# Performance work log

Hardware: AMD Instinct MI355X
Metric: run time of the kernel (lower is better)

The kernel has to match this reference:

```python
import jax, jax.numpy as jnp
import numpy as np

B, S, H, D = 1, 8192, 16, 128
BS = 64            # sparse_block_size
NB = S // BS       # 128 blocks
NUM_ORACLES = 32
ORACLE = S // NUM_ORACLES          # 256
LOCAL = ORACLE // BS               # 4 sliding-window blocks
PATTERN_ID = 0


def _build_block_pattern():
    """Block-level mask exactly as DKernelPredefinedSparseAttention.create_mask((0,))."""
    qb = np.arange(NB)[:, None]
    kb = np.arange(NB)[None, :]
    causal = qb >= kb
    window = (qb - kb) < LOCAL
    vert = np.zeros(NB, dtype=bool)
    real_col = int(PATTERN_ID * ORACLE + 0.5)
    vert[real_col // BS:(real_col + ORACLE) // BS] = True
    vert[0:1] = True
    mask = causal & (window | vert[None, :])
    kmax = int(mask.sum(axis=1).max())  # = 8 for this pattern
    kidx = np.zeros((NB, kmax), dtype=np.int32)
    kvalid = np.zeros((NB, kmax), dtype=bool)
    for i in range(NB):
        idx = np.nonzero(mask[i])[0]
        kidx[i, :len(idx)] = idx
        kvalid[i, :len(idx)] = True
    return kidx, kvalid


def setup_inputs() -> dict:
    key = jax.random.key(0)
    kq, kk, kv = jax.random.split(key, 3)
    q = jax.random.normal(kq, (B, S, H, D), dtype=jnp.float32)
    k = jax.random.normal(kk, (B, S, H, D), dtype=jnp.float32)
    v = jax.random.normal(kv, (B, S, H, D), dtype=jnp.float32)
    kidx_np, kvalid_np = _build_block_pattern()
    return {"q": q, "k": k, "v": v,
            "kidx": jnp.asarray(kidx_np), "kvalid": jnp.asarray(kvalid_np)}


def reference(q, k, v, kidx, kvalid):
    # q,k,v: [B,S,H,D] (bshd). kidx/kvalid: [NB, Kmax] active k-block ids per q-block.
    b, s, h, d = q.shape
    nb = s // BS
    kmax = kidx.shape[1]
    qb = q.reshape(b, nb, BS, h, d)
    kb = k.reshape(b, nb, BS, h, d)
    vb = v.reshape(b, nb, BS, h, d)
    # Gather only active k/v blocks -> [B, nb, Kmax, BS, H, D]
    kg = kb[:, kidx]
    vg = vb[:, kidx]
    scale = 1.0 / jnp.sqrt(jnp.float32(d))
    # [B, H, nb, BS(q), Kmax, BS(k)]
    scores = jnp.einsum('bqahd,bqkchd->bhqakc', qb, kg) * scale
    # element-level causal mask within the block pattern
    qpos = jnp.arange(nb)[:, None] * BS + jnp.arange(BS)[None, :]          # [nb, BS]
    kpos = kidx[..., None] * BS + jnp.arange(BS)[None, None, :]            # [nb, Kmax, BS]
    allow = (qpos[:, :, None, None] >= kpos[:, None, :, :]) & kvalid[:, None, :, None]
    scores = jnp.where(allow[None, None], scores, jnp.float32(-1e30))
    probs = jax.nn.softmax(scores.reshape(b, h, nb, BS, kmax * BS), axis=-1)
    probs = probs.reshape(scores.shape)
    out = jnp.einsum('bhqakc,bqkchd->bqahd', probs, vg)
    return out.reshape(b, s, h, d)
```

## Files before the change

### kernel.cpp

```cpp
#include <hip/hip_runtime.h>
#include <hip/hip_bf16.h>

#define HH 16
#define DD 128
#define NBQ 128
#define SS 8192

typedef __attribute__((ext_vector_type(4))) float f32x4;
typedef __attribute__((ext_vector_type(4))) short bf16x4;
typedef __attribute__((ext_vector_type(8))) short bf16x8;

__device__ __forceinline__ short f2bf_hw(float f) {
  __hip_bfloat16 b = __float2bfloat16(f);
  return __builtin_bit_cast(short, b);
}

__device__ __forceinline__ void gload_lds16(const void* g, void* l) {
  __builtin_amdgcn_global_load_lds(
      (const __attribute__((address_space(1))) void*)g,
      (__attribute__((address_space(3))) void*)l, 16, 0, 0);
}

__global__ __launch_bounds__(256)
void conv_k_kernel(const float* __restrict__ kg, unsigned short* __restrict__ kb) {
  const size_t e = ((size_t)blockIdx.x * 256 + threadIdx.x) * 4;
  const int h = (int)(e >> 20);
  const int s = (int)((e >> 7) & (SS - 1));
  const int d = (int)(e & 127);
  f32x4 a = *(const f32x4*)(kg + ((size_t)s * HH + h) * DD + d);
  bf16x4 o;
  o[0] = f2bf_hw(a[0]); o[1] = f2bf_hw(a[1]);
  o[2] = f2bf_hw(a[2]); o[3] = f2bf_hw(a[3]);
  *(bf16x4*)(kb + e) = o;
}

__global__ __launch_bounds__(256)
void conv_vt2_kernel(const float* __restrict__ vg, unsigned short* __restrict__ vt) {
  __shared__ unsigned short tile[128 * 72];
  const int kb = blockIdx.x, h = blockIdx.y, tid = threadIdx.x;
  {
    const int r = tid >> 2, q = tid & 3;
    const float* vp = vg + ((size_t)(kb * 64 + r) * HH + h) * DD + q * 32;
    #pragma unroll
    for (int c = 0; c < 8; ++c) {
      f32x4 a = *(const f32x4*)(vp + c * 4);
      #pragma unroll
      for (int j = 0; j < 4; ++j)
        tile[(q * 32 + c * 4 + j) * 72 + r] = (unsigned short)f2bf_hw(a[j]);
    }
  }
  __syncthreads();
  const int d = tid >> 1, half = tid & 1;
  unsigned short* op = vt + ((size_t)(h * NBQ + kb) * 128 + d) * 64 + half * 32;
  #pragma unroll
  for (int j = 0; j < 4; ++j) {
    bf16x8 f;
    #pragma unroll
    for (int e = 0; e < 8; ++e) {
      const int p = half * 32 + j * 8 + e;
      const int key = ((p >> 2) & 3) * 16 + (p >> 4) * 4 + (p & 3);
      f[e] = (short)tile[d * 72 + key];
    }
    *(bf16x8*)(op + j * 8) = f;
  }
}

#define SWK(o) ((o) ^ ((((o) >> 8) & 7) << 4))
#define SWV(o) ((o) ^ ((((o) >> 7) & 7) << 4))

__global__ __launch_bounds__(512, 4)
void sparse_attn_v14(const float* __restrict__ qg_, const unsigned short* __restrict__ kbuf,
                     const unsigned short* __restrict__ vtbuf, float* __restrict__ outg) {
  extern __shared__ __align__(16) char lds[];

  const int bx   = blockIdx.x;
  const int w    = (bx & 7) * 128 + (bx >> 3);
  const int h    = w >> 6;
  const int qgrp = w & 63;
  const int tid  = threadIdx.x;
  const int wid  = tid >> 6;
  const int lane = tid & 63;
  const int l15  = lane & 15;
  const int lg   = lane >> 4;

  const int qlo  = qgrp * 2, qhi = qgrp * 2 + 1;
  const int qb_w = qlo + (wid >> 2);
  const int rib0 = (wid & 3) * 16;

  const int nv     = (qhi + 1 < 4) ? qhi + 1 : 4;
  const int wstart = (qlo - 3 > 4) ? qlo - 3 : 4;
  const int nw     = (qhi - wstart + 1 > 0) ? qhi - wstart + 1 : 0;
  const int nlist  = nv + nw;

  const float scale = 0.12752030522080552f;

  const int rowg = qgrp * 128 + (wid >> 2) * 64 + rib0;

  bf16x8 qa[4];
  {
    const float* qp = qg_ + ((size_t)(rowg + l15) * HH + h) * DD;
    #pragma unroll
    for (int kc = 0; kc < 4; ++kc) {
      const int d0 = kc * 32 + lg * 8;
      f32x4 a = *(const f32x4*)(qp + d0);
      f32x4 b = *(const f32x4*)(qp + d0 + 4);
      bf16x8 f;
      f[0] = f2bf_hw(a[0] * scale); f[1] = f2bf_hw(a[1] * scale);
      f[2] = f2bf_hw(a[2] * scale); f[3] = f2bf_hw(a[3] * scale);
      f[4] = f2bf_hw(b[0] * scale); f[5] = f2bf_hw(b[1] * scale);
      f[6] = f2bf_hw(b[2] * scale); f[7] = f2bf_hw(b[3] * scale);
      qa[kc] = f;
    }
  }

  f32x4 oa[8];
  #pragma unroll
  for (int i = 0; i < 8; ++i) oa[i] = (f32x4){0.f, 0.f, 0.f, 0.f};
  float mr = -1e30f;
  float lr = 0.f;

  const char* kbase = (const char*)kbuf + ((size_t)h * NBQ << 14);
  const char* vbase = (const char*)vtbuf + ((size_t)h * NBQ << 14);

  {
    #pragma unroll
    for (int p = 0; p < 2; ++p) {
      const int ob = p * 8192 + wid * 1024;
      const int o  = ob + lane * 16;
      gload_lds16(kbase + SWK(o), lds + ob);
      gload_lds16(vbase + SWV(o), lds + 16384 + ob);
    }
  }
  __syncthreads();

  for (int t = 0; t < nlist; ++t) {
    const int kb = (t < nv) ? t : (wstart + (t - nv));
    const bool valid = (kb <= qb_w) && ((qb_w - kb < 4) || (kb < 4));
    char* Vb = lds + 16384 + (t & 1) * 16384;
    const bool havenext = (t + 1 < nlist);
    const int kbn = havenext ? ((t + 1 < nv) ? (t + 1) : (wstart + (t + 1 - nv))) : 0;

    if (havenext) {
      const char* vsrc = vbase + ((size_t)kbn << 14);
      char* Vd = lds + 16384 + ((t + 1) & 1) * 16384;
      #pragma unroll
      for (int p = 0; p < 2; ++p) {
        const int ob = p * 8192 + wid * 1024;
        const int o  = ob + lane * 16;
        gload_lds16(vsrc + SWV(o), Vd + ob);
      }
    }

    f32x4 s[4];
    if (valid) {
      #pragma unroll
      for (int kt = 0; kt < 4; ++kt) s[kt] = (f32x4){0.f, 0.f, 0.f, 0.f};
      __builtin_amdgcn_s_setprio(1);
      #pragma unroll
      for (int kt = 0; kt < 4; ++kt) {
        const int key = kt * 16 + l15;
        #pragma unroll
        for (int kc = 0; kc < 4; ++kc) {
          const int off = (key * 256 + (kc * 32 + lg * 8) * 2) ^ ((key & 7) << 4);
          bf16x8 kf = *(const bf16x8*)(lds + off);
          s[kt] = __builtin_amdgcn_mfma_f32_16x16x32_bf16(kf, qa[kc], s[kt], 0, 0, 0);
        }
      }
      __builtin_amdgcn_s_setprio(0);
    }

    __syncthreads();

    if (havenext) {
      const char* ksrc = kbase + ((size_t)kbn << 14);
      #pragma unroll
      for (int p = 0; p < 2; ++p) {
        const int ob = p * 8192 + wid * 1024;
        const int o  = ob + lane * 16;
        gload_lds16(ksrc + SWK(o), lds + ob);
      }
    }

    if (valid) {
      if (kb == qb_w) {
        const int rib = rib0 + l15;
        #pragma unroll
        for (int kt = 0; kt < 4; ++kt)
          #pragma unroll
          for (int r = 0; r < 4; ++r) {
            const int key = kt * 16 + lg * 4 + r;
            if (rib < key) s[kt][r] = -1e30f;
          }
      }

      {
        float a0 = fmaxf(fmaxf(s[0][0], s[0][1]), fmaxf(s[0][2], s[0][3]));
        float a1 = fmaxf(fmaxf(s[1][0], s[1][1]), fmaxf(s[1][2], s[1][3]));
        float a2 = fmaxf(fmaxf(s[2][0], s[2][1]), fmaxf(s[2][2], s[2][3]));
        float a3 = fmaxf(fmaxf(s[3][0], s[3][1]), fmaxf(s[3][2], s[3][3]));
        float lanemax = fmaxf(fmaxf(a0, a1), fmaxf(a2, a3));
        if (!__all(lanemax <= mr + 8.f)) {
          float mx = lanemax;
          mx = fmaxf(mx, __shfl_xor(mx, 16));
          mx = fmaxf(mx, __shfl_xor(mx, 32));
          const float mnew = fmaxf(mr, mx);
          const float sc = __builtin_amdgcn_exp2f(mr - mnew);
          lr *= sc;
          mr = mnew;
          const float s0 = __shfl(sc, lg * 4 + 0);
          const float s1 = __shfl(sc, lg * 4 + 1);
          const float s2 = __shfl(sc, lg * 4 + 2);
          const float s3 = __shfl(sc, lg * 4 + 3);
          #pragma unroll
          for (int nd = 0; nd < 8; ++nd) {
            oa[nd][0] *= s0; oa[nd][1] *= s1;
            oa[nd][2] *= s2; oa[nd][3] *= s3;
          }
        }
        float lsum = 0.f;
        #pragma unroll
        for (int kt = 0; kt < 4; ++kt)
          #pragma unroll
          for (int r = 0; r < 4; ++r) {
            const float p = __builtin_amdgcn_exp2f(s[kt][r] - mr);
            s[kt][r] = p;
            lsum += p;
          }
        lr += lsum;
      }

      bf16x4 pa[4];
      #pragma unroll
      for (int kt = 0; kt < 4; ++kt) {
        unsigned u0 = (unsigned)(unsigned short)f2bf_hw(s[kt][0]) |
                      ((unsigned)(unsigned short)f2bf_hw(s[kt][1]) << 16);
        unsigned u1 = (unsigned)(unsigned short)f2bf_hw(s[kt][2]) |
                      ((unsigned)(unsigned short)f2bf_hw(s[kt][3]) << 16);
        uint2 uu; uu.x = u0; uu.y = u1;
        pa[kt] = __builtin_bit_cast(bf16x4, uu);
      }

      __builtin_amdgcn_s_setprio(1);
      #pragma unroll
      for (int nd = 0; nd < 8; ++nd) {
        const int d = nd * 16 + l15;
        #pragma unroll
        for (int hb = 0; hb < 2; ++hb) {
          const int off = (d * 128 + lg * 32 + hb * 16) ^ ((d & 7) << 4);
          bf16x8 v2 = *(const bf16x8*)(Vb + off);
          bf16x4 vlo = __builtin_shufflevector(v2, v2, 0, 1, 2, 3);
          bf16x4 vhi = __builtin_shufflevector(v2, v2, 4, 5, 6, 7);
          oa[nd] = __builtin_amdgcn_mfma_f32_16x16x16bf16_1k(pa[2 * hb],     vlo, oa[nd], 0, 0, 0);
          oa[nd] = __builtin_amdgcn_mfma_f32_16x16x16bf16_1k(pa[2 * hb + 1], vhi, oa[nd], 0, 0, 0);
        }
      }
      __builtin_amdgcn_s_setprio(0);
    }
    __syncthreads();
  }

  {
    float l = lr;
    l += __shfl_xor(l, 16);
    l += __shfl_xor(l, 32);
    const float inv = 1.0f / l;
    const float i0 = __shfl(inv, lg * 4 + 0);
    const float i1 = __shfl(inv, lg * 4 + 1);
    const float i2 = __shfl(inv, lg * 4 + 2);
    const float i3 = __shfl(inv, lg * 4 + 3);
    float* op = outg + ((size_t)rowg * HH + h) * DD;
    #pragma unroll
    for (int nd = 0; nd < 8; ++nd) {
      const int d = nd * 16 + l15;
      op[(size_t)(lg * 4 + 0) * HH * DD + d] = oa[nd][0] * i0;
      op[(size_t)(lg * 4 + 1) * HH * DD + d] = oa[nd][1] * i1;
      op[(size_t)(lg * 4 + 2) * HH * DD + d] = oa[nd][2] * i2;
      op[(size_t)(lg * 4 + 3) * HH * DD + d] = oa[nd][3] * i3;
    }
  }
}

extern "C" void kernel_launch(void* const* d_in, const int* in_sizes, int n_in,
                              void* d_out, int out_size, void* d_ws, size_t ws_size,
                              hipStream_t stream) {
  const float* q = (const float*)d_in[0];
  const float* k = (const float*)d_in[1];
  const float* v = (const float*)d_in[2];
  float* out = (float*)d_out;
  const size_t elems = (size_t)HH * SS * DD;
  unsigned short* kbuf  = (unsigned short*)d_ws;
  unsigned short* vtbuf = kbuf + elems;

  conv_k_kernel<<<(int)(elems / 4 / 256), 256, 0, stream>>>(k, kbuf);
  conv_vt2_kernel<<<dim3(NBQ, HH), 256, 0, stream>>>(v, vtbuf);
  sparse_attn_v14<<<dim3(NBQ / 2 * HH), 512, 49152, stream>>>(q, kbuf, vtbuf, out);
}
```

Measured before the change: 113.0 us.

## Double-buffer K tiles and use explicit vmcnt waits with raw barriers

K is now double-buffered in LDS like V, so the next K and V blocks are prefetched together at the top of each iteration. One mid-loop __syncthreads goes away, and __syncthreads is replaced by raw s_barrier plus manual s_waitcnt vmcnt(4), so the current tile's loads can be waited on while the prefetch stays in flight. This reduces per-iteration synchronisation and increases overlap. In exchange, LDS per block rises from 48KB to 64KB, which can reduce occupancy, and the manual vmcnt counting relies on async LDS-load accounting being correct.

Result: faster. 109.6 us (-3.1%).

```diff
diff --git a/kernel.cpp b/kernel.cpp
--- a/kernel.cpp
+++ b/kernel.cpp
@@ -19,6 +19,12 @@
   __builtin_amdgcn_global_load_lds(
       (const __attribute__((address_space(1))) void*)g,
       (__attribute__((address_space(3))) void*)l, 16, 0, 0);
+}
+
+__device__ __forceinline__ void wg_barrier() {
+  asm volatile("" ::: "memory");
+  __builtin_amdgcn_s_barrier();
+  asm volatile("" ::: "memory");
 }
 
 __global__ __launch_bounds__(256)
@@ -69,7 +75,7 @@
 #define SWV(o) ((o) ^ ((((o) >> 7) & 7) << 4))
 
 __global__ __launch_bounds__(512, 4)
-void sparse_attn_v14(const float* __restrict__ qg_, const unsigned short* __restrict__ kbuf,
+void sparse_attn_v15(const float* __restrict__ qg_, const unsigned short* __restrict__ kbuf,
                      const unsigned short* __restrict__ vtbuf, float* __restrict__ outg) {
   extern __shared__ __align__(16) char lds[];
 
@@ -121,38 +127,52 @@
 
   const char* kbase = (const char*)kbuf + ((size_t)h * NBQ << 14);
   const char* vbase = (const char*)vtbuf + ((size_t)h * NBQ << 14);
+  const int o0 = wid * 1024 + lane * 16;
 
   {
     #pragma unroll
     for (int p = 0; p < 2; ++p) {
-      const int ob = p * 8192 + wid * 1024;
-      const int o  = ob + lane * 16;
-      gload_lds16(kbase + SWK(o), lds + ob);
-      gload_lds16(vbase + SWV(o), lds + 16384 + ob);
-    }
-  }
-  __syncthreads();
+      const int o = p * 8192 + o0;
+      gload_lds16(kbase + SWK(o), lds + o - lane * 16 + lane * 16);
+    }
+    #pragma unroll
+    for (int p = 0; p < 2; ++p) {
+      const int o = p * 8192 + o0;
+      gload_lds16(vbase + SWV(o), lds + 32768 + o - lane * 16 + lane * 16);
+    }
+  }
 
   for (int t = 0; t < nlist; ++t) {
     const int kb = (t < nv) ? t : (wstart + (t - nv));
     const bool valid = (kb <= qb_w) && ((qb_w - kb < 4) || (kb < 4));
-    char* Vb = lds + 16384 + (t & 1) * 16384;
+    char* Kb = lds + (t & 1) * 16384;
+    char* Vb = lds + 32768 + (t & 1) * 16384;
     const bool havenext = (t + 1 < nlist);
-    const int kbn = havenext ? ((t + 1 < nv) ? (t + 1) : (wstart + (t + 1 - nv))) : 0;
 
     if (havenext) {
+      const int kbn = (t + 1 < nv) ? (t + 1) : (wstart + (t + 1 - nv));
+      const char* ksrc = kbase + ((size_t)kbn << 14);
       const char* vsrc = vbase + ((size_t)kbn << 14);
-      char* Vd = lds + 16384 + ((t + 1) & 1) * 16384;
+      char* Kd = lds + ((t + 1) & 1) * 16384;
+      char* Vd = lds + 32768 + ((t + 1) & 1) * 16384;
       #pragma unroll
       for (int p = 0; p < 2; ++p) {
-        const int ob = p * 8192 + wid * 1024;
-        const int o  = ob + lane * 16;
-        gload_lds16(vsrc + SWV(o), Vd + ob);
-      }
-    }
-
-    f32x4 s[4];
+        const int o = p * 8192 + o0;
+        gload_lds16(ksrc + SWK(o), Kd + p * 8192 + wid * 1024);
+      }
+      #pragma unroll
+      for (int p = 0; p < 2; ++p) {
+        const int o = p * 8192 + o0;
+        gload_lds16(vsrc + SWV(o), Vd + p * 8192 + wid * 1024);
+      }
+      asm volatile("s_waitcnt vmcnt(4)" ::: "memory");
+    } else {
+      asm volatile("s_waitcnt vmcnt(0)" ::: "memory");
+    }
+    wg_barrier();
+
     if (valid) {
+      f32x4 s[4];
       #pragma unroll
       for (int kt = 0; kt < 4; ++kt) s[kt] = (f32x4){0.f, 0.f, 0.f, 0.f};
       __builtin_amdgcn_s_setprio(1);
@@ -162,26 +182,12 @@
         #pragma unroll
         for (int kc = 0; kc < 4; ++kc) {
           const int off = (key * 256 + (kc * 32 + lg * 8) * 2) ^ ((key & 7) << 4);
-          bf16x8 kf = *(const bf16x8*)(lds + off);
+          bf16x8 kf = *(const bf16x8*)(Kb + off);
           s[kt] = __builtin_amdgcn_mfma_f32_16x16x32_bf16(kf, qa[kc], s[kt], 0, 0, 0);
         }
       }
       __builtin_amdgcn_s_setprio(0);
-    }
-
-    __syncthreads();
-
-    if (havenext) {
-      const char* ksrc = kbase + ((size_t)kbn << 14);
-      #pragma unroll
-      for (int p = 0; p < 2; ++p) {
-        const int ob = p * 8192 + wid * 1024;
-        const int o  = ob + lane * 16;
-        gload_lds16(ksrc + SWK(o), lds + ob);
-      }
-    }
-
-    if (valid) {
+
       if (kb == qb_w) {
         const int rib = rib0 + l15;
         #pragma unroll
@@ -256,7 +262,7 @@
       }
       __builtin_amdgcn_s_setprio(0);
     }
-    __syncthreads();
+    wg_barrier();
   }
 
   {
@@ -293,5 +299,5 @@
 
   conv_k_kernel<<<(int)(elems / 4 / 256), 256, 0, stream>>>(k, kbuf);
   conv_vt2_kernel<<<dim3(NBQ, HH), 256, 0, stream>>>(v, vtbuf);
-  sparse_attn_v14<<<dim3(NBQ / 2 * HH), 512, 49152, stream>>>(q, kbuf, vtbuf, out);
-}
+  sparse_attn_v15<<<dim3(NBQ / 2 * HH), 512, 65536, stream>>>(q, kbuf, vtbuf, out);
+}
```

## Fuse K fp32-to-bf16 conversion into attention kernel with double-buffered K

Applied to the files above, without the earlier changes.

Drops the separate K conversion pre-pass. The attention kernel now loads fp32 K straight from global memory into registers, converts it to bf16, and writes it swizzled into a double-buffered K region in LDS. One mid-loop __syncthreads is removed because K now has two buffers. This saves a kernel launch and a full write/read round-trip of K. In exchange it raises LDS use to 64KB per block, which may cut occupancy, and holds the prefetched K in registers across the QK MFMA.

Result: slower. 153.2 us (+35.5%).

```diff
diff --git a/kernel.cpp b/kernel.cpp
--- a/kernel.cpp
+++ b/kernel.cpp
@@ -19,19 +19,6 @@
   __builtin_amdgcn_global_load_lds(
       (const __attribute__((address_space(1))) void*)g,
       (__attribute__((address_space(3))) void*)l, 16, 0, 0);
-}
-
-__global__ __launch_bounds__(256)
-void conv_k_kernel(const float* __restrict__ kg, unsigned short* __restrict__ kb) {
-  const size_t e = ((size_t)blockIdx.x * 256 + threadIdx.x) * 4;
-  const int h = (int)(e >> 20);
-  const int s = (int)((e >> 7) & (SS - 1));
-  const int d = (int)(e & 127);
-  f32x4 a = *(const f32x4*)(kg + ((size_t)s * HH + h) * DD + d);
-  bf16x4 o;
-  o[0] = f2bf_hw(a[0]); o[1] = f2bf_hw(a[1]);
-  o[2] = f2bf_hw(a[2]); o[3] = f2bf_hw(a[3]);
-  *(bf16x4*)(kb + e) = o;
 }
 
 __global__ __launch_bounds__(256)
@@ -69,7 +56,7 @@
 #define SWV(o) ((o) ^ ((((o) >> 7) & 7) << 4))
 
 __global__ __launch_bounds__(512, 4)
-void sparse_attn_v14(const float* __restrict__ qg_, const unsigned short* __restrict__ kbuf,
+void sparse_attn_v17(const float* __restrict__ qg_, const float* __restrict__ kg,
                      const unsigned short* __restrict__ vtbuf, float* __restrict__ outg) {
   extern __shared__ __align__(16) char lds[];
 
@@ -119,16 +106,30 @@
   float mr = -1e30f;
   float lr = 0.f;
 
-  const char* kbase = (const char*)kbuf + ((size_t)h * NBQ << 14);
+  const int kkey = tid >> 3;
+  const int kd0  = (tid & 7) * 16;
+  const int kob0 = SWK(tid * 32);
+  const int kob1 = SWK(tid * 32 + 16);
   const char* vbase = (const char*)vtbuf + ((size_t)h * NBQ << 14);
+  const int vo0 = wid * 1024 + lane * 16;
 
   {
+    const float* kp = kg + (((size_t)(0 * 64 + kkey)) * HH + h) * DD + kd0;
+    f32x4 ka = *(const f32x4*)(kp);
+    f32x4 kb_ = *(const f32x4*)(kp + 4);
+    f32x4 kc = *(const f32x4*)(kp + 8);
+    f32x4 kd = *(const f32x4*)(kp + 12);
+    bf16x8 w0, w1;
+    w0[0] = f2bf_hw(ka[0]); w0[1] = f2bf_hw(ka[1]); w0[2] = f2bf_hw(ka[2]); w0[3] = f2bf_hw(ka[3]);
+    w0[4] = f2bf_hw(kb_[0]); w0[5] = f2bf_hw(kb_[1]); w0[6] = f2bf_hw(kb_[2]); w0[7] = f2bf_hw(kb_[3]);
+    w1[0] = f2bf_hw(kc[0]); w1[1] = f2bf_hw(kc[1]); w1[2] = f2bf_hw(kc[2]); w1[3] = f2bf_hw(kc[3]);
+    w1[4] = f2bf_hw(kd[0]); w1[5] = f2bf_hw(kd[1]); w1[6] = f2bf_hw(kd[2]); w1[7] = f2bf_hw(kd[3]);
+    *(bf16x8*)(lds + kob0) = w0;
+    *(bf16x8*)(lds + kob1) = w1;
     #pragma unroll
     for (int p = 0; p < 2; ++p) {
-      const int ob = p * 8192 + wid * 1024;
-      const int o  = ob + lane * 16;
-      gload_lds16(kbase + SWK(o), lds + ob);
-      gload_lds16(vbase + SWV(o), lds + 16384 + ob);
+      const int o = p * 8192 + vo0;
+      gload_lds16(vbase + SWV(o), lds + 32768 + p * 8192 + wid * 1024);
     }
   }
   __syncthreads();
@@ -136,18 +137,24 @@
   for (int t = 0; t < nlist; ++t) {
     const int kb = (t < nv) ? t : (wstart + (t - nv));
     const bool valid = (kb <= qb_w) && ((qb_w - kb < 4) || (kb < 4));
-    char* Vb = lds + 16384 + (t & 1) * 16384;
+    char* Kb = lds + (t & 1) * 16384;
+    char* Vb = lds + 32768 + (t & 1) * 16384;
     const bool havenext = (t + 1 < nlist);
     const int kbn = havenext ? ((t + 1 < nv) ? (t + 1) : (wstart + (t + 1 - nv))) : 0;
 
+    f32x4 ks0, ks1, ks2, ks3;
     if (havenext) {
+      const float* kp = kg + (((size_t)(kbn * 64 + kkey)) * HH + h) * DD + kd0;
+      ks0 = *(const f32x4*)(kp);
+      ks1 = *(const f32x4*)(kp + 4);
+      ks2 = *(const f32x4*)(kp + 8);
+      ks3 = *(const f32x4*)(kp + 12);
       const char* vsrc = vbase + ((size_t)kbn << 14);
-      char* Vd = lds + 16384 + ((t + 1) & 1) * 16384;
+      char* Vd = lds + 32768 + ((t + 1) & 1) * 16384;
       #pragma unroll
       for (int p = 0; p < 2; ++p) {
-        const int ob = p * 8192 + wid * 1024;
-        const int o  = ob + lane * 16;
-        gload_lds16(vsrc + SWV(o), Vd + ob);
+        const int o = p * 8192 + vo0;
+        gload_lds16(vsrc + SWV(o), Vd + p * 8192 + wid * 1024);
       }
     }
 
@@ -162,23 +169,22 @@
         #pragma unroll
         for (int kc = 0; kc < 4; ++kc) {
           const int off = (key * 256 + (kc * 32 + lg * 8) * 2) ^ ((key & 7) << 4);
-          bf16x8 kf = *(const bf16x8*)(lds + off);
+          bf16x8 kf = *(const bf16x8*)(Kb + off);
           s[kt] = __builtin_amdgcn_mfma_f32_16x16x32_bf16(kf, qa[kc], s[kt], 0, 0, 0);
         }
       }
       __builtin_amdgcn_s_setprio(0);
     }
 
-    __syncthreads();
-
     if (havenext) {
-      const char* ksrc = kbase + ((size_t)kbn << 14);
-      #pragma unroll
-      for (int p = 0; p < 2; ++p) {
-        const int ob = p * 8192 + wid * 1024;
-        const int o  = ob + lane * 16;
-        gload_lds16(ksrc + SWK(o), lds + ob);
-      }
+      char* Kd = lds + ((t + 1) & 1) * 16384;
+      bf16x8 w0, w1;
+      w0[0] = f2bf_hw(ks0[0]); w0[1] = f2bf_hw(ks0[1]); w0[2] = f2bf_hw(ks0[2]); w0[3] = f2bf_hw(ks0[3]);
+      w0[4] = f2bf_hw(ks1[0]); w0[5] = f2bf_hw(ks1[1]); w0[6] = f2bf_hw(ks1[2]); w0[7] = f2bf_hw(ks1[3]);
+      w1[0] = f2bf_hw(ks2[0]); w1[1] = f2bf_hw(ks2[1]); w1[2] = f2bf_hw(ks2[2]); w1[3] = f2bf_hw(ks2[3]);
+      w1[4] = f2bf_hw(ks3[0]); w1[5] = f2bf_hw(ks3[1]); w1[6] = f2bf_hw(ks3[2]); w1[7] = f2bf_hw(ks3[3]);
+      *(bf16x8*)(Kd + kob0) = w0;
+      *(bf16x8*)(Kd + kob1) = w1;
     }
 
     if (valid) {
@@ -287,11 +293,8 @@
   const float* k = (const float*)d_in[1];
   const float* v = (const float*)d_in[2];
   float* out = (float*)d_out;
-  const size_t elems = (size_t)HH * SS * DD;
-  unsigned short* kbuf  = (unsigned short*)d_ws;
-  unsigned short* vtbuf = kbuf + elems;
-
-  conv_k_kernel<<<(int)(elems / 4 / 256), 256, 0, stream>>>(k, kbuf);
+  unsigned short* vtbuf = (unsigned short*)d_ws;
+
   conv_vt2_kernel<<<dim3(NBQ, HH), 256, 0, stream>>>(v, vtbuf);
-  sparse_attn_v14<<<dim3(NBQ / 2 * HH), 512, 49152, stream>>>(q, kbuf, vtbuf, out);
-}
+  sparse_attn_v17<<<dim3(NBQ / 2 * HH), 512, 65536, stream>>>(q, k, vtbuf, out);
+}
```
